# Performance work log

Measured on AMD Instinct MI355X. Metric: run time of the kernel, lower is better.

## Reference

```python
import jax, jax.numpy as jnp
import numpy as np

DIM = 1024
HEADS = 16

def setup_inputs() -> dict:
    key = jax.random.key(0)
    ks = jax.random.split(key, 9)
    s = DIM ** -0.5  # init scale for weights
    x = jax.random.normal(ks[0], (2, 2048, DIM), dtype=jnp.float32)
    wq = jax.random.normal(ks[1], (DIM, DIM), dtype=jnp.float32) * s
    bq = jax.random.normal(ks[2], (DIM,), dtype=jnp.float32) * 0.01
    wk = jax.random.normal(ks[3], (DIM, DIM), dtype=jnp.float32) * s
    bk = jax.random.normal(ks[4], (DIM,), dtype=jnp.float32) * 0.01
    wv = jax.random.normal(ks[5], (DIM, DIM), dtype=jnp.float32) * s
    bv = jax.random.normal(ks[6], (DIM,), dtype=jnp.float32) * 0.01
    wo = jax.random.normal(ks[7], (DIM, DIM), dtype=jnp.float32) * s
    bo = jax.random.normal(ks[8], (DIM,), dtype=jnp.float32) * 0.01
    return {"x": x, "wq": wq, "bq": bq, "wk": wk, "bk": bk,
            "wv": wv, "bv": bv, "wo": wo, "bo": bo}

def reference(x, wq, bq, wk, bk, wv, bv, wo, bo):
    b, l, dim = x.shape
    h = HEADS
    d = dim // h
    scale = dim ** -0.5  # NOTE: full dim, as in the original module
    # torch Linear: x @ W.T + b
    def proj(w, bias):
        y = jnp.einsum('bld,ed->ble', x, w) + bias
        return y.reshape(b, l, h, d).transpose(0, 2, 1, 3)  # b h l d
    q = proj(wq, bq)
    k = proj(wk, bk)
    v = proj(wv, bv)
    attn = jnp.einsum('bhid,bhjd->bhij', q, k) * scale
    attn = jax.nn.softmax(attn, axis=-1)
    out = jnp.einsum('bhij,bhjd->bhid', attn, v)
    out = out.transpose(0, 2, 1, 3).reshape(b, l, dim)
    return jnp.einsum('ble,fe->blf', out, wo) + bo
```

## Files before the change

kernel.cpp:

```cpp
#include <hip/hip_runtime.h>
#include <hip/hip_bf16.h>
#include <stdint.h>


typedef __attribute__((ext_vector_type(8))) short short8;
typedef __attribute__((ext_vector_type(4))) float f32x4;
typedef __attribute__((ext_vector_type(16))) float f32x16;

#define MFMA(a, b, c) __builtin_amdgcn_mfma_f32_16x16x32_bf16((a), (b), (c), 0, 0, 0)
#define MFMA32(a, b, c) __builtin_amdgcn_mfma_f32_32x32x16_bf16((a), (b), (c), 0, 0, 0)

#if __has_builtin(__builtin_amdgcn_exp2f)
#define EXP2(x) __builtin_amdgcn_exp2f(x)
#else
#define EXP2(x) exp2f(x)
#endif

__device__ __forceinline__ ushort f2bf(float f) {
  uint32_t u = __builtin_bit_cast(uint32_t, f);
  u += 0x7fffu + ((u >> 16) & 1u);
  return (ushort)(u >> 16);
}

__device__ __forceinline__ uint32_t cvtpk(float lo, float hi) {
  uint32_t u;
  asm("v_cvt_pk_bf16_f32 %0, %1, %2" : "=v"(u) : "v"(lo), "v"(hi));
  return u;
}

__device__ __forceinline__ void pl32swap(uint32_t& a, uint32_t& b) {
  asm("v_permlane32_swap_b32 %0, %1" : "+v"(a), "+v"(b));
}

__device__ __forceinline__ void gl_lds16(const void* g, void* l) {
  __builtin_amdgcn_global_load_lds(
      (const __attribute__((address_space(1))) unsigned int*)g,
      (__attribute__((address_space(3))) unsigned int*)l, 16, 0, 0);
}

__global__ __launch_bounds__(256) void convert_all(
    const float* __restrict__ x, const float* __restrict__ wq,
    const float* __restrict__ wk, const float* __restrict__ wv,
    const float* __restrict__ wo, ushort* __restrict__ dst) {
  size_t i4 = (size_t)blockIdx.x * 256 + threadIdx.x;
  size_t e = i4 * 4;
  const float* src; size_t off;
  if (e < 4194304u)      { src = x;  off = e; }
  else if (e < 5242880u) { src = wq; off = e - 4194304u; }
  else if (e < 6291456u) { src = wk; off = e - 5242880u; }
  else if (e < 7340032u) { src = wv; off = e - 6291456u; }
  else                   { src = wo; off = e - 7340032u; }
  float4 v = *(const float4*)(src + off);
  ushort4 o = { f2bf(v.x), f2bf(v.y), f2bf(v.z), f2bf(v.w) };
  *(ushort4*)(dst + e) = o;
}

__global__ __launch_bounds__(256) void gemm_qkv(
    const ushort* __restrict__ xb,
    const ushort* __restrict__ wqb, const ushort* __restrict__ wkb,
    const ushort* __restrict__ wvb,
    const float* __restrict__ bq_, const float* __restrict__ bk_,
    const float* __restrict__ bv_,
    ushort* __restrict__ qout, ushort* __restrict__ kout,
    ushort* __restrict__ vtout) {
  __shared__ __align__(16) ushort As[128 * 32];
  __shared__ __align__(16) ushort Bs[128 * 32];
  const int wg = blockIdx.x;
  const int l = (wg & 7) * 96 + (wg >> 3);
  const int bn = l & 7, bm = (l >> 3) & 31, z = l >> 8;
  const int t = threadIdx.x;
  const int w = t >> 6, lane = t & 63;
  const int wr = w >> 1, wc = w & 1;
  const int l15 = lane & 15, l4 = lane >> 4;

  const ushort* wb = (z == 0) ? wqb : (z == 1 ? wkb : wvb);
  const float* bias = (z == 0) ? bq_ : (z == 1 ? bk_ : bv_);

  f32x4 acc[4][4] = {};

  for (int kt = 0; kt < 32; ++kt) {
    __syncthreads();
#pragma unroll
    for (int rr = 0; rr < 2; ++rr) {
      int c = t + rr * 256;
      int row = c >> 2, cin = c & 3;
      gl_lds16(xb + (bm * 128 + row) * 1024 + kt * 32 + cin * 8, (void*)&As[c * 8]);
      gl_lds16(wb + (bn * 128 + row) * 1024 + kt * 32 + cin * 8, (void*)&Bs[c * 8]);
    }
    __syncthreads();
    short8 af[4], bfr[4];
#pragma unroll
    for (int mf = 0; mf < 4; ++mf)
      af[mf] = *(const short8*)&As[(wr * 64 + mf * 16 + l15) * 32 + l4 * 8];
#pragma unroll
    for (int nf = 0; nf < 4; ++nf)
      bfr[nf] = *(const short8*)&Bs[(wc * 64 + nf * 16 + l15) * 32 + l4 * 8];
    __builtin_amdgcn_s_setprio(1);
#pragma unroll
    for (int mf = 0; mf < 4; ++mf)
#pragma unroll
      for (int nf = 0; nf < 4; ++nf)
        acc[mf][nf] = MFMA(af[mf], bfr[nf], acc[mf][nf]);
    __builtin_amdgcn_s_setprio(0);
  }

  const float qsc = 0.045084439f;
#pragma unroll
  for (int mf = 0; mf < 4; ++mf) {
#pragma unroll
    for (int nf = 0; nf < 4; ++nf) {
      int n = bn * 128 + wc * 64 + nf * 16 + l15;
      int m0 = bm * 128 + wr * 64 + mf * 16 + l4 * 4;
      float b = bias[n];
      float vals[4];
#pragma unroll
      for (int r = 0; r < 4; ++r) vals[r] = acc[mf][nf][r] + b;
      int bb = m0 >> 11, l0 = m0 & 2047;
      int h = n >> 6, d = n & 63;
      int bh = bb * 16 + h;
      if (z == 2) {
        *(uint2*)&vtout[(bh * 64 + d) * 2048 + l0] =
            make_uint2(cvtpk(vals[0], vals[1]), cvtpk(vals[2], vals[3]));
      } else if (z == 0) {
#pragma unroll
        for (int r = 0; r < 4; ++r)
          qout[(bh * 2048 + l0 + r) * 64 + d] = f2bf(vals[r] * qsc);
      } else {
#pragma unroll
        for (int r = 0; r < 4; ++r)
          kout[(bh * 2048 + l0 + r) * 64 + d] = f2bf(vals[r]);
      }
    }
  }
}

__global__ __launch_bounds__(256, 2) void attn(
    const ushort* __restrict__ qb, const ushort* __restrict__ kb,
    const ushort* __restrict__ vtb, ushort* __restrict__ aout) {
  __shared__ __align__(16) ushort Ks[4][64 * 64];
  __shared__ __align__(16) ushort Vs[4][64 * 64];
  const int bid = blockIdx.x;
  const int xcd = bid & 7, idx = bid >> 3;
  const int bh = xcd * 4 + (idx >> 4);
  const int it = idx & 15;
  const int t = threadIdx.x, w = t >> 6, lane = t & 63;
  const int l31 = lane & 31, hi = lane >> 5;
  const size_t kvbase = (size_t)bh * (2048 * 64);
  const int i0 = it * 128 + w * 32;

  const int c0 = t, c1 = t + 256;
  const int r0 = c0 >> 3, s0 = (c0 & 7) ^ (r0 & 7);
  const int r1 = c1 >> 3, s1 = (c1 & 7) ^ (r1 & 7);

#define STAGE(bufi, jts)                                                     \
  {                                                                          \
    const int j0s = (jts) * 64;                                              \
    gl_lds16(kb + kvbase + (size_t)(j0s + r0) * 64 + s0 * 8,                 \
             (void*)&Ks[bufi][c0 * 8]);                                      \
    gl_lds16(kb + kvbase + (size_t)(j0s + r1) * 64 + s1 * 8,                 \
             (void*)&Ks[bufi][c1 * 8]);                                      \
    gl_lds16(vtb + kvbase + (size_t)r0 * 2048 + j0s + s0 * 8,                \
             (void*)&Vs[bufi][c0 * 8]);                                      \
    gl_lds16(vtb + kvbase + (size_t)r1 * 2048 + j0s + s1 * 8,                \
             (void*)&Vs[bufi][c1 * 8]);                                      \
  }

#define QKSTEP(kbuf)                                                         \
  {                                                                          \
    const ushort* Kc = &Ks[kbuf][0];                                         \
    __builtin_amdgcn_s_setprio(1);                                           \
    _Pragma("unroll")                                                        \
    for (int ks = 0; ks < 4; ++ks) {                                         \
      int ck = (ks * 2 + hi) ^ swz;                                          \
      short8 a0 = *(const short8*)&Kc[l31 * 64 + ck * 8];                    \
      short8 a1 = *(const short8*)&Kc[(32 + l31) * 64 + ck * 8];             \
      st0 = MFMA32(a0, qf[ks], st0);                                         \
      st1 = MFMA32(a1, qf[ks], st1);                                         \
    }                                                                        \
    __builtin_amdgcn_s_setprio(0);                                           \
  }

  short8 qf[4];
#pragma unroll
  for (int ks = 0; ks < 4; ++ks)
    qf[ks] = *(const short8*)&qb[kvbase + (size_t)(i0 + l31) * 64 + ks * 16 + hi * 8];

  f32x16 ot0 = {}, ot1 = {};
  float ts0 = 0.f, ts1 = 0.f, ts2 = 0.f, ts3 = 0.f;
  const int swz = (l31 & 7);

  STAGE(0, 0);
  STAGE(1, 1);
  asm volatile("s_waitcnt vmcnt(4)" ::: "memory");
  __builtin_amdgcn_s_barrier();
  asm volatile("" ::: "memory");

  f32x16 st0 = {}, st1 = {};
  QKSTEP(0);

  for (int jt = 0; jt < 32; ++jt) {
    const int cur = jt & 3;
    STAGE((jt + 2) & 3, (jt + 2 < 32) ? (jt + 2) : 31);

    const ushort* Vc = &Vs[cur][0];
    short8 va0[4], va1[4];
#pragma unroll
    for (int b = 0; b < 4; ++b) {
      int cv = (b * 2 + hi) ^ swz;
      va0[b] = *(const short8*)&Vc[l31 * 64 + cv * 8];
      va1[b] = *(const short8*)&Vc[(32 + l31) * 64 + cv * 8];
    }

    f32x16 p0, p1;
#pragma unroll
    for (int r = 0; r < 16; r += 4) {
      p0[r] = EXP2(st0[r]);         ts0 += p0[r];
      p0[r + 1] = EXP2(st0[r + 1]); ts1 += p0[r + 1];
      p0[r + 2] = EXP2(st0[r + 2]); ts2 += p0[r + 2];
      p0[r + 3] = EXP2(st0[r + 3]); ts3 += p0[r + 3];
    }
#pragma unroll
    for (int r = 0; r < 16; r += 4) {
      p1[r] = EXP2(st1[r]);         ts0 += p1[r];
      p1[r + 1] = EXP2(st1[r + 1]); ts1 += p1[r + 1];
      p1[r + 2] = EXP2(st1[r + 2]); ts2 += p1[r + 2];
      p1[r + 3] = EXP2(st1[r + 3]); ts3 += p1[r + 3];
    }

    short8 pb[4];
#pragma unroll
    for (int b = 0; b < 4; ++b) {
      f32x16 pv = (b < 2) ? p0 : p1;
      const int R = 8 * (b & 1);
      uint32_t c01 = cvtpk(pv[R + 0], pv[R + 1]);
      uint32_t c23 = cvtpk(pv[R + 2], pv[R + 3]);
      uint32_t c45 = cvtpk(pv[R + 4], pv[R + 5]);
      uint32_t c67 = cvtpk(pv[R + 6], pv[R + 7]);
      pl32swap(c01, c45);
      pl32swap(c23, c67);
      union { uint32_t u[4]; short8 s; } pk;
      pk.u[0] = c01; pk.u[1] = c23; pk.u[2] = c45; pk.u[3] = c67;
      pb[b] = pk.s;
    }

    __builtin_amdgcn_s_setprio(1);
#pragma unroll
    for (int b = 0; b < 4; ++b) {
      ot0 = MFMA32(va0[b], pb[b], ot0);
      ot1 = MFMA32(va1[b], pb[b], ot1);
    }
    __builtin_amdgcn_s_setprio(0);

    asm volatile("s_waitcnt vmcnt(4)" ::: "memory");
    __builtin_amdgcn_s_barrier();
    asm volatile("" ::: "memory");

    if (jt < 31) {
#pragma unroll
      for (int r = 0; r < 16; ++r) { st0[r] = 0.f; st1[r] = 0.f; }
      QKSTEP((jt + 1) & 3);
    }
  }

  float lsum = (ts0 + ts1) + (ts2 + ts3);
  {
    uint32_t a = __builtin_bit_cast(uint32_t, lsum);
    uint32_t b = a;
    pl32swap(a, b);
    lsum = __builtin_bit_cast(float, a) + __builtin_bit_cast(float, b);
  }
  const int bb = bh >> 4, h = bh & 15;
  float inv = 1.0f / lsum;
  ushort* orow = aout + (size_t)(bb * 2048 + i0 + l31) * 1024 + h * 64;
#pragma unroll
  for (int mf = 0; mf < 2; ++mf) {
    f32x16 o = mf ? ot1 : ot0;
#pragma unroll
    for (int g = 0; g < 4; ++g) {
      int d0 = mf * 32 + g * 8 + hi * 4;
      *(uint2*)(orow + d0) = make_uint2(
          cvtpk(o[g * 4 + 0] * inv, o[g * 4 + 1] * inv),
          cvtpk(o[g * 4 + 2] * inv, o[g * 4 + 3] * inv));
    }
  }
#undef STAGE
#undef QKSTEP
}

__global__ __launch_bounds__(256) void gemm_out(
    const ushort* __restrict__ ab, const ushort* __restrict__ wob,
    const float* __restrict__ bo_, float* __restrict__ out) {
  __shared__ __align__(16) ushort As[128 * 32];
  __shared__ __align__(16) ushort Bs[128 * 32];
  const int wg = blockIdx.x;
  const int l = (wg & 7) * 32 + (wg >> 3);
  const int bn = l & 7, bm = l >> 3;
  const int t = threadIdx.x;
  const int w = t >> 6, lane = t & 63;
  const int wr = w >> 1, wc = w & 1;
  const int l15 = lane & 15, l4 = lane >> 4;

  f32x4 acc[4][4] = {};

  for (int kt = 0; kt < 32; ++kt) {
    __syncthreads();
#pragma unroll
    for (int rr = 0; rr < 2; ++rr) {
      int c = t + rr * 256;
      int row = c >> 2, cin = c & 3;
      gl_lds16(ab + (bm * 128 + row) * 1024 + kt * 32 + cin * 8, (void*)&As[c * 8]);
      gl_lds16(wob + (bn * 128 + row) * 1024 + kt * 32 + cin * 8, (void*)&Bs[c * 8]);
    }
    __syncthreads();
    short8 af[4], bfr[4];
#pragma unroll
    for (int mf = 0; mf < 4; ++mf)
      af[mf] = *(const short8*)&As[(wr * 64 + mf * 16 + l15) * 32 + l4 * 8];
#pragma unroll
    for (int nf = 0; nf < 4; ++nf)
      bfr[nf] = *(const short8*)&Bs[(wc * 64 + nf * 16 + l15) * 32 + l4 * 8];
    __builtin_amdgcn_s_setprio(1);
#pragma unroll
    for (int mf = 0; mf < 4; ++mf)
#pragma unroll
      for (int nf = 0; nf < 4; ++nf)
        acc[mf][nf] = MFMA(af[mf], bfr[nf], acc[mf][nf]);
    __builtin_amdgcn_s_setprio(0);
  }

#pragma unroll
  for (int mf = 0; mf < 4; ++mf)
#pragma unroll
    for (int nf = 0; nf < 4; ++nf) {
      int n = bn * 128 + wc * 64 + nf * 16 + l15;
      int m0 = bm * 128 + wr * 64 + mf * 16 + l4 * 4;
      float b = bo_[n];
#pragma unroll
      for (int r = 0; r < 4; ++r)
        out[(size_t)(m0 + r) * 1024 + n] = acc[mf][nf][r] + b;
    }
}

extern "C" void kernel_launch(void* const* d_in, const int* in_sizes, int n_in,
                              void* d_out, int out_size, void* d_ws, size_t ws_size,
                              hipStream_t stream) {
  const float* x  = (const float*)d_in[0];
  const float* wq = (const float*)d_in[1];
  const float* bq = (const float*)d_in[2];
  const float* wk = (const float*)d_in[3];
  const float* bk = (const float*)d_in[4];
  const float* wv = (const float*)d_in[5];
  const float* bv = (const float*)d_in[6];
  const float* wo = (const float*)d_in[7];
  const float* bo = (const float*)d_in[8];

  ushort* ws  = (ushort*)d_ws;
  ushort* xb  = ws;
  ushort* wqb = ws + 4194304;
  ushort* wkb = ws + 5242880;
  ushort* wvb = ws + 6291456;
  ushort* wob = ws + 7340032;
  ushort* qbp = ws + 8388608;
  ushort* kbp = ws + 12582912;
  ushort* vtb = ws + 16777216;
  ushort* ab  = ws + 20971520;

  convert_all<<<8192, 256, 0, stream>>>(x, wq, wk, wv, wo, ws);
  gemm_qkv<<<768, 256, 0, stream>>>(xb, wqb, wkb, wvb, bq, bk, bv,
                                    qbp, kbp, vtb);
  attn<<<512, 256, 0, stream>>>(qbp, kbp, vtb, ab);
  gemm_out<<<256, 256, 0, stream>>>(ab, wob, bo, (float*)d_out);
}
```

Before: 113.8 us.

## Double per-wave query rows in attention to reuse K/V fragments

Each attention wave now handles 64 query rows (two 32-row groups) instead of 32, so each K and V fragment read from LDS feeds twice as many MFMAs. The grid halves from 512 to 256 blocks and launch bounds drop to one block per CU to make room for the doubled accumulators. This cuts LDS reads and global K/V staging traffic per query row. In exchange it raises register pressure, lowers occupancy, and leaves only 256 blocks for the 256 CUs, so there is less latency hiding.

```diff
diff --git a/kernel.cpp b/kernel.cpp
--- a/kernel.cpp
+++ b/kernel.cpp
@@ -134,19 +134,19 @@
   }
 }
 
-__global__ __launch_bounds__(256, 2) void attn(
+__global__ __launch_bounds__(256, 1) void attn(
     const ushort* __restrict__ qb, const ushort* __restrict__ kb,
     const ushort* __restrict__ vtb, ushort* __restrict__ aout) {
   __shared__ __align__(16) ushort Ks[4][64 * 64];
   __shared__ __align__(16) ushort Vs[4][64 * 64];
   const int bid = blockIdx.x;
   const int xcd = bid & 7, idx = bid >> 3;
-  const int bh = xcd * 4 + (idx >> 4);
-  const int it = idx & 15;
+  const int bh = xcd * 4 + (idx >> 3);
+  const int it = idx & 7;
   const int t = threadIdx.x, w = t >> 6, lane = t & 63;
   const int l31 = lane & 31, hi = lane >> 5;
   const size_t kvbase = (size_t)bh * (2048 * 64);
-  const int i0 = it * 128 + w * 32;
+  const int i0w = it * 256 + w * 64;
 
   const int c0 = t, c1 = t + 256;
   const int r0 = c0 >> 3, s0 = (c0 & 7) ^ (r0 & 7);
@@ -174,19 +174,56 @@
       int ck = (ks * 2 + hi) ^ swz;                                          \
       short8 a0 = *(const short8*)&Kc[l31 * 64 + ck * 8];                    \
       short8 a1 = *(const short8*)&Kc[(32 + l31) * 64 + ck * 8];             \
-      st0 = MFMA32(a0, qf[ks], st0);                                         \
-      st1 = MFMA32(a1, qf[ks], st1);                                         \
+      st00 = MFMA32(a0, qf0[ks], st00);                                      \
+      st01 = MFMA32(a1, qf0[ks], st01);                                      \
+      st10 = MFMA32(a0, qf1[ks], st10);                                      \
+      st11 = MFMA32(a1, qf1[ks], st11);                                      \
     }                                                                        \
     __builtin_amdgcn_s_setprio(0);                                           \
   }
 
-  short8 qf[4];
-#pragma unroll
-  for (int ks = 0; ks < 4; ++ks)
-    qf[ks] = *(const short8*)&qb[kvbase + (size_t)(i0 + l31) * 64 + ks * 16 + hi * 8];
-
-  f32x16 ot0 = {}, ot1 = {};
-  float ts0 = 0.f, ts1 = 0.f, ts2 = 0.f, ts3 = 0.f;
+#define SOFTMAX_RG(stA, stB, pbX, tsX)                                       \
+  {                                                                          \
+    f32x16 p0, p1;                                                           \
+    _Pragma("unroll")                                                        \
+    for (int r = 0; r < 16; r += 4) {                                        \
+      p0[r] = EXP2(stA[r]);         tsX[0] += p0[r];                         \
+      p0[r + 1] = EXP2(stA[r + 1]); tsX[1] += p0[r + 1];                     \
+      p0[r + 2] = EXP2(stA[r + 2]); tsX[2] += p0[r + 2];                     \
+      p0[r + 3] = EXP2(stA[r + 3]); tsX[3] += p0[r + 3];                     \
+    }                                                                        \
+    _Pragma("unroll")                                                        \
+    for (int r = 0; r < 16; r += 4) {                                        \
+      p1[r] = EXP2(stB[r]);         tsX[0] += p1[r];                         \
+      p1[r + 1] = EXP2(stB[r + 1]); tsX[1] += p1[r + 1];                     \
+      p1[r + 2] = EXP2(stB[r + 2]); tsX[2] += p1[r + 2];                     \
+      p1[r + 3] = EXP2(stB[r + 3]); tsX[3] += p1[r + 3];                     \
+    }                                                                        \
+    _Pragma("unroll")                                                        \
+    for (int b = 0; b < 4; ++b) {                                            \
+      f32x16 pv = (b < 2) ? p0 : p1;                                         \
+      const int R = 8 * (b & 1);                                             \
+      uint32_t c01 = cvtpk(pv[R + 0], pv[R + 1]);                            \
+      uint32_t c23 = cvtpk(pv[R + 2], pv[R + 3]);                            \
+      uint32_t c45 = cvtpk(pv[R + 4], pv[R + 5]);                            \
+      uint32_t c67 = cvtpk(pv[R + 6], pv[R + 7]);                            \
+      pl32swap(c01, c45);                                                    \
+      pl32swap(c23, c67);                                                    \
+      union { uint32_t u[4]; short8 s; } pk;                                 \
+      pk.u[0] = c01; pk.u[1] = c23; pk.u[2] = c45; pk.u[3] = c67;            \
+      pbX[b] = pk.s;                                                         \
+    }                                                                        \
+  }
+
+  short8 qf0[4], qf1[4];
+#pragma unroll
+  for (int ks = 0; ks < 4; ++ks) {
+    qf0[ks] = *(const short8*)&qb[kvbase + (size_t)(i0w + l31) * 64 + ks * 16 + hi * 8];
+    qf1[ks] = *(const short8*)&qb[kvbase + (size_t)(i0w + 32 + l31) * 64 + ks * 16 + hi * 8];
+  }
+
+  f32x16 ot00 = {}, ot01 = {}, ot10 = {}, ot11 = {};
+  float ts0[4] = {}, ts1[4] = {};
   const int swz = (l31 & 7);
 
   STAGE(0, 0);
@@ -195,59 +232,28 @@
   __builtin_amdgcn_s_barrier();
   asm volatile("" ::: "memory");
 
-  f32x16 st0 = {}, st1 = {};
+  f32x16 st00 = {}, st01 = {}, st10 = {}, st11 = {};
   QKSTEP(0);
 
   for (int jt = 0; jt < 32; ++jt) {
     const int cur = jt & 3;
     STAGE((jt + 2) & 3, (jt + 2 < 32) ? (jt + 2) : 31);
 
+    short8 pb0[4], pb1[4];
+    SOFTMAX_RG(st00, st01, pb0, ts0);
+    SOFTMAX_RG(st10, st11, pb1, ts1);
+
     const ushort* Vc = &Vs[cur][0];
-    short8 va0[4], va1[4];
+    __builtin_amdgcn_s_setprio(1);
 #pragma unroll
     for (int b = 0; b < 4; ++b) {
       int cv = (b * 2 + hi) ^ swz;
-      va0[b] = *(const short8*)&Vc[l31 * 64 + cv * 8];
-      va1[b] = *(const short8*)&Vc[(32 + l31) * 64 + cv * 8];
-    }
-
-    f32x16 p0, p1;
-#pragma unroll
-    for (int r = 0; r < 16; r += 4) {
-      p0[r] = EXP2(st0[r]);         ts0 += p0[r];
-      p0[r + 1] = EXP2(st0[r + 1]); ts1 += p0[r + 1];
-      p0[r + 2] = EXP2(st0[r + 2]); ts2 += p0[r + 2];
-      p0[r + 3] = EXP2(st0[r + 3]); ts3 += p0[r + 3];
-    }
-#pragma unroll
-    for (int r = 0; r < 16; r += 4) {
-      p1[r] = EXP2(st1[r]);         ts0 += p1[r];
-      p1[r + 1] = EXP2(st1[r + 1]); ts1 += p1[r + 1];
-      p1[r + 2] = EXP2(st1[r + 2]); ts2 += p1[r + 2];
-      p1[r + 3] = EXP2(st1[r + 3]); ts3 += p1[r + 3];
-    }
-
-    short8 pb[4];
-#pragma unroll
-    for (int b = 0; b < 4; ++b) {
-      f32x16 pv = (b < 2) ? p0 : p1;
-      const int R = 8 * (b & 1);
-      uint32_t c01 = cvtpk(pv[R + 0], pv[R + 1]);
-      uint32_t c23 = cvtpk(pv[R + 2], pv[R + 3]);
-      uint32_t c45 = cvtpk(pv[R + 4], pv[R + 5]);
-      uint32_t c67 = cvtpk(pv[R + 6], pv[R + 7]);
-      pl32swap(c01, c45);
-      pl32swap(c23, c67);
-      union { uint32_t u[4]; short8 s; } pk;
-      pk.u[0] = c01; pk.u[1] = c23; pk.u[2] = c45; pk.u[3] = c67;
-      pb[b] = pk.s;
-    }
-
-    __builtin_amdgcn_s_setprio(1);
-#pragma unroll
-    for (int b = 0; b < 4; ++b) {
-      ot0 = MFMA32(va0[b], pb[b], ot0);
-      ot1 = MFMA32(va1[b], pb[b], ot1);
+      short8 va0 = *(const short8*)&Vc[l31 * 64 + cv * 8];
+      short8 va1 = *(const short8*)&Vc[(32 + l31) * 64 + cv * 8];
+      ot00 = MFMA32(va0, pb0[b], ot00);
+      ot01 = MFMA32(va1, pb0[b], ot01);
+      ot10 = MFMA32(va0, pb1[b], ot10);
+      ot11 = MFMA32(va1, pb1[b], ot11);
     }
     __builtin_amdgcn_s_setprio(0);
 
@@ -257,34 +263,40 @@
 
     if (jt < 31) {
 #pragma unroll
-      for (int r = 0; r < 16; ++r) { st0[r] = 0.f; st1[r] = 0.f; }
+      for (int r = 0; r < 16; ++r) {
+        st00[r] = 0.f; st01[r] = 0.f; st10[r] = 0.f; st11[r] = 0.f;
+      }
       QKSTEP((jt + 1) & 3);
     }
   }
 
-  float lsum = (ts0 + ts1) + (ts2 + ts3);
-  {
+  const int bb = bh >> 4, h = bh & 15;
+#pragma unroll
+  for (int rg = 0; rg < 2; ++rg) {
+    float lsum = rg ? ((ts1[0] + ts1[1]) + (ts1[2] + ts1[3]))
+                    : ((ts0[0] + ts0[1]) + (ts0[2] + ts0[3]));
     uint32_t a = __builtin_bit_cast(uint32_t, lsum);
-    uint32_t b = a;
-    pl32swap(a, b);
-    lsum = __builtin_bit_cast(float, a) + __builtin_bit_cast(float, b);
-  }
-  const int bb = bh >> 4, h = bh & 15;
-  float inv = 1.0f / lsum;
-  ushort* orow = aout + (size_t)(bb * 2048 + i0 + l31) * 1024 + h * 64;
-#pragma unroll
-  for (int mf = 0; mf < 2; ++mf) {
-    f32x16 o = mf ? ot1 : ot0;
+    uint32_t b2 = a;
+    pl32swap(a, b2);
+    lsum = __builtin_bit_cast(float, a) + __builtin_bit_cast(float, b2);
+    float inv = 1.0f / lsum;
+    int i = i0w + rg * 32 + l31;
+    ushort* orow = aout + (size_t)(bb * 2048 + i) * 1024 + h * 64;
+    f32x16 oA = rg ? ot10 : ot00;
+    f32x16 oB = rg ? ot11 : ot01;
 #pragma unroll
     for (int g = 0; g < 4; ++g) {
-      int d0 = mf * 32 + g * 8 + hi * 4;
-      *(uint2*)(orow + d0) = make_uint2(
-          cvtpk(o[g * 4 + 0] * inv, o[g * 4 + 1] * inv),
-          cvtpk(o[g * 4 + 2] * inv, o[g * 4 + 3] * inv));
+      *(uint2*)(orow + g * 8 + hi * 4) = make_uint2(
+          cvtpk(oA[g * 4 + 0] * inv, oA[g * 4 + 1] * inv),
+          cvtpk(oA[g * 4 + 2] * inv, oA[g * 4 + 3] * inv));
+      *(uint2*)(orow + 32 + g * 8 + hi * 4) = make_uint2(
+          cvtpk(oB[g * 4 + 0] * inv, oB[g * 4 + 1] * inv),
+          cvtpk(oB[g * 4 + 2] * inv, oB[g * 4 + 3] * inv));
     }
   }
 #undef STAGE
 #undef QKSTEP
+#undef SOFTMAX_RG
 }
 
 __global__ __launch_bounds__(256) void gemm_out(
@@ -368,6 +380,6 @@
   convert_all<<<8192, 256, 0, stream>>>(x, wq, wk, wv, wo, ws);
   gemm_qkv<<<768, 256, 0, stream>>>(xb, wqb, wkb, wvb, bq, bk, bv,
                                     qbp, kbp, vtb);
-  attn<<<512, 256, 0, stream>>>(qbp, kbp, vtb, ab);
+  attn<<<256, 256, 0, stream>>>(qbp, kbp, vtb, ab);
   gemm_out<<<256, 256, 0, stream>>>(ab, wob, bo, (float*)d_out);
 }
```

New measurement: 118.2 us. 1.04x slower.
